# Performance work log

Hardware: AMD Instinct MI355X
Metric: run time of the kernel (lower is better)

## Reference

```python
import jax, jax.numpy as jnp
from jax import lax
import numpy as np

MAX_ITER = 50
BAND_WIDTH = 3.0
MIN_BAND_VOXELS = 32
EPS = 1e-06


def _chamfer(mask_f):
    # mask_f: [N, H, W] float in {0,1}. Iterative 3x3 max-pool dilation; a pixel
    # newly reached at iteration i gets distance i (matches torch max_pool2d loop).
    # Running the full MAX_ITER iterations is equivalent to the early break:
    # once no new pixels appear, dist is never updated again.
    def body(i, carry):
        dist, cur = carry
        dil = lax.reduce_window(cur, -jnp.inf, lax.max, (1, 3, 3), (1, 1, 1), 'SAME')
        new = (dil > 0) & (cur == 0)
        dist = jnp.where(new, i.astype(dist.dtype), dist)
        return (dist, dil)

    dist0 = jnp.zeros_like(mask_f)
    dist, _ = lax.fori_loop(1, MAX_ITER + 1, body, (dist0, mask_f))
    return dist


def _signed_distance(m):
    # m: [N, H, W] float binary masks. Positive outside, negative inside.
    H, W = m.shape[-2], m.shape[-1]
    sdm = _chamfer(m) - _chamfer(1.0 - m)
    msum = m.sum((-2, -1))
    trivial = (msum == 0) | (msum == H * W)  # all-empty or all-full -> zeros
    return jnp.where(trivial[:, None, None], 0.0, sdm)


def setup_inputs() -> dict:
    key = jax.random.key(0)
    k1, k2 = jax.random.split(key)
    B, C, H, W = 8, 4, 512, 512
    probs = jax.random.uniform(k1, (B, C, H, W), dtype=jnp.float32)
    target = jax.random.randint(k2, (B, H, W), 0, C, dtype=jnp.int64)
    return {"probs": probs, "target": target}


def reference(probs, target):
    B, C, H, W = probs.shape
    probs = probs.astype(jnp.float32)
    # one-hot [B, C, H, W] bool; default include_background=False -> classes 1..C-1
    one_hot = target[:, None, :, :] == jnp.arange(C, dtype=target.dtype)[None, :, None, None]
    m = one_hot[:, 1:].astype(jnp.float32).reshape(B * (C - 1), H, W)
    p = probs[:, 1:].reshape(B * (C - 1), H, W)

    d = jnp.abs(_signed_distance(m))          # [N, H, W]
    band = (d <= BAND_WIDTH).astype(jnp.float32)
    denom = band.sum((-2, -1))                 # [N]

    err = jnp.abs(p - m)                       # L1 (error_power=1.0)
    loss_bc = (err * d * band).sum((-2, -1)) / (denom + EPS)

    include = (denom >= MIN_BAND_VOXELS).astype(jnp.float32)
    count = include.sum()
    return (loss_bc * include).sum() / (count + EPS)
```

## Files before the change

kernel.cpp:

```cpp
#include <hip/hip_runtime.h>


#define HH 512
#define WW 512
#define BB 8
#define NCLS 4
#define TILE 32
#define HALO 3
#define LTS (TILE + 2*HALO)
#define LSTRIDE 40
#define NBLK 2048
#define WS2_OFF (9 * NBLK)


__global__ __launch_bounds__(256) void gsl_stage1(
    const float* __restrict__ probs,
    const int*   __restrict__ target,
    float* __restrict__ ws)
{
    __shared__ uint32_t tile[LTS * LSTRIDE];
    __shared__ float redf[4][3];
    __shared__ int   redi[4][3];

    const int b   = blockIdx.z;
    const int gx0 = blockIdx.x * TILE - HALO;
    const int gy0 = blockIdx.y * TILE - HALO;
    const int tid = threadIdx.y * 16 + threadIdx.x;
    const int* __restrict__ tgt_b = target + b * (HH * WW);

    for (int i = tid; i < LTS * LTS; i += 256) {
        int ly = i / LTS, lx = i - ly * LTS;
        int gy = gy0 + ly, gx = gx0 + lx;
        uint32_t bits = 0u;
        if ((unsigned)gy < (unsigned)HH && (unsigned)gx < (unsigned)WW)
            bits = 1u << (uint32_t)tgt_b[gy * WW + gx];
        tile[ly * LSTRIDE + lx] = bits;
    }
    __syncthreads();

    float num[3] = {0.f, 0.f, 0.f};
    int   den[3] = {0, 0, 0};
    int   mc [3] = {0, 0, 0};

    #pragma unroll
    for (int sy = 0; sy < 2; ++sy)
    #pragma unroll
    for (int sx = 0; sx < 2; ++sx) {
        const int px = threadIdx.x + 16 * sx;
        const int py = threadIdx.y + 16 * sy;
        const int lx = px + HALO, ly = py + HALO;
        const int gx = blockIdx.x * TILE + px;
        const int gy = blockIdx.y * TILE + py;

        uint32_t p1 = 0u, p2 = 0u, p3 = 0u;
        #pragma unroll
        for (int dy = -3; dy <= 3; ++dy) {
            #pragma unroll
            for (int dx = -3; dx <= 3; ++dx) {
                uint32_t v = tile[(ly + dy) * LSTRIDE + (lx + dx)];
                const int ady = dy < 0 ? -dy : dy;
                const int adx = dx < 0 ? -dx : dx;
                const int r = ady > adx ? ady : adx;
                if (r <= 1) p1 |= v;
                if (r <= 2) p2 |= v;
                p3 |= v;
            }
        }
        const uint32_t cbits = tile[ly * LSTRIDE + lx];

        #pragma unroll
        for (int k = 0; k < 3; ++k) {
            const int c = k + 1;
            const uint32_t cm = 1u << c;
            const bool v = (cbits & cm) != 0u;
            const bool a1 = v ? ((p1 & ~cm) != 0u) : ((p1 & cm) != 0u);
            const bool a2 = v ? ((p2 & ~cm) != 0u) : ((p2 & cm) != 0u);
            const bool a3 = v ? ((p3 & ~cm) != 0u) : ((p3 & cm) != 0u);
            const int d = a1 ? 1 : (a2 ? 2 : 3);
            const float p = probs[(((b * NCLS) + c) * HH + gy) * WW + gx];
            const float err = fabsf(p - (v ? 1.0f : 0.0f));
            num[k] += a3 ? err * (float)d : 0.0f;
            den[k] += a3 ? 1 : 0;
            mc [k] += v ? 1 : 0;
        }
    }

    int pk0 = den[0] | (den[1] << 16);
    int pk1 = den[2] | (mc[0] << 16);
    int pk2 = mc[1]  | (mc[2] << 16);

    const int lane = tid & 63, wave = tid >> 6;
    #pragma unroll
    for (int off = 32; off; off >>= 1) {
        num[0] += __shfl_down(num[0], off, 64);
        num[1] += __shfl_down(num[1], off, 64);
        num[2] += __shfl_down(num[2], off, 64);
        pk0    += __shfl_down(pk0,    off, 64);
        pk1    += __shfl_down(pk1,    off, 64);
        pk2    += __shfl_down(pk2,    off, 64);
    }
    if (lane == 0) {
        redf[wave][0] = num[0]; redf[wave][1] = num[1]; redf[wave][2] = num[2];
        redi[wave][0] = pk0;    redi[wave][1] = pk1;    redi[wave][2] = pk2;
    }
    __syncthreads();
    if (tid == 0) {
        const int blockFlat = ((b * 16) + blockIdx.y) * 16 + blockIdx.x;
        float n0 = 0.f, n1 = 0.f, n2 = 0.f;
        int s0 = 0, s1 = 0, s2 = 0;
        #pragma unroll
        for (int w = 0; w < 4; ++w) {
            n0 += redf[w][0]; n1 += redf[w][1]; n2 += redf[w][2];
            s0 += redi[w][0]; s1 += redi[w][1]; s2 += redi[w][2];
        }
        ws[(0 * 3 + 0) * NBLK + blockFlat] = n0;
        ws[(0 * 3 + 1) * NBLK + blockFlat] = n1;
        ws[(0 * 3 + 2) * NBLK + blockFlat] = n2;
        ws[(1 * 3 + 0) * NBLK + blockFlat] = (float)(s0 & 0xFFFF);
        ws[(1 * 3 + 1) * NBLK + blockFlat] = (float)(s0 >> 16);
        ws[(1 * 3 + 2) * NBLK + blockFlat] = (float)(s1 & 0xFFFF);
        ws[(2 * 3 + 0) * NBLK + blockFlat] = (float)(s1 >> 16);
        ws[(2 * 3 + 1) * NBLK + blockFlat] = (float)(s2 & 0xFFFF);
        ws[(2 * 3 + 2) * NBLK + blockFlat] = (float)(s2 >> 16);
    }
}

__global__ __launch_bounds__(256) void gsl_stage2(float* __restrict__ ws)
{
    __shared__ float red[4];
    const int g = blockIdx.x;
    const int k = g >> 3, b = g & 7;
    const int tid = threadIdx.x;

    float s = ws[k * NBLK + b * 256 + tid];
    #pragma unroll
    for (int off = 32; off; off >>= 1) s += __shfl_down(s, off, 64);
    if ((tid & 63) == 0) red[tid >> 6] = s;
    __syncthreads();
    if (tid == 0) {
        const int grp = k / 3, cc = k % 3;
        ws[WS2_OFF + grp * 24 + b * 3 + cc] = red[0] + red[1] + red[2] + red[3];
    }
}

__global__ __launch_bounds__(64) void gsl_stage3(
    const float* __restrict__ ws, float* __restrict__ out)
{
    const float* ws2 = ws + WS2_OFF;
    const int n = threadIdx.x;
    float loss = 0.0f, incl = 0.0f;
    if (n < 24) {
        const float num = ws2[n];
        const float den = ws2[24 + n];
        const float mcv = ws2[48 + n];
        const bool trivial = (mcv == 0.0f) || (mcv == (float)(HH * WW));
        if (trivial) {
            incl = 1.0f; loss = 0.0f;
        } else if (den >= 32.0f) {
            incl = 1.0f;
            loss = num / (den + 1e-6f);
        }
    }
    #pragma unroll
    for (int off = 32; off; off >>= 1) {
        loss += __shfl_down(loss, off, 64);
        incl += __shfl_down(incl, off, 64);
    }
    if (n == 0) out[0] = loss / (incl + 1e-6f);
}

extern "C" void kernel_launch(void* const* d_in, const int* in_sizes, int n_in,
                              void* d_out, int out_size, void* d_ws, size_t ws_size,
                              hipStream_t stream)
{
    const float* probs  = (const float*)d_in[0];
    const int*   target = (const int*)d_in[1];
    float* out = (float*)d_out;
    float* ws  = (float*)d_ws;

    dim3 grid1(WW / TILE, HH / TILE, BB);
    dim3 block1(16, 16);
    gsl_stage1<<<grid1, block1, 0, stream>>>(probs, target, ws);
    gsl_stage2<<<72, 256, 0, stream>>>(ws);
    gsl_stage3<<<1, 64, 0, stream>>>(ws, out);
}
```

Baseline: 94.57 us.

## Pack class bitmasks into nibbles and compute band distances with row-wise dilation

Replaces the 2D shared-memory tile with 7x7 neighbourhood ORs by packing 8 pixels' class bits into one 32-bit word per lane. Horizontal 1/2/3-pixel dilations are built with shifts and cross-lane shuffles, and vertical dilation is an OR over rows stored in shared memory. Blocks now process full-width 8-row strips with vectorized int4/float4 loads, and the two reduction kernels are merged into one finishing kernel. The aim is to cut the 49 LDS reads per pixel, the halo overhead and one kernel launch. The cost is more complex bit logic and fewer, larger blocks (512 total).

```diff
diff --git a/kernel.cpp b/kernel.cpp
--- a/kernel.cpp
+++ b/kernel.cpp
@@ -4,13 +4,9 @@
 #define HH 512
 #define WW 512
 #define BB 8
-#define NCLS 4
-#define TILE 32
-#define HALO 3
-#define LTS (TILE + 2*HALO)
-#define LSTRIDE 40
-#define NBLK 2048
-#define WS2_OFF (9 * NBLK)
+#define STRIP 8
+#define SROWS (STRIP + 6)
+#define NBLK 512
 
 
 __global__ __launch_bounds__(256) void gsl_stage1(
@@ -18,23 +14,40 @@
     const int*   __restrict__ target,
     float* __restrict__ ws)
 {
-    __shared__ uint32_t tile[LTS * LSTRIDE];
+    __shared__ uint4 hrow[SROWS * 64];
     __shared__ float redf[4][3];
     __shared__ int   redi[4][3];
 
-    const int b   = blockIdx.z;
-    const int gx0 = blockIdx.x * TILE - HALO;
-    const int gy0 = blockIdx.y * TILE - HALO;
-    const int tid = threadIdx.y * 16 + threadIdx.x;
+    const int tid   = threadIdx.x;
+    const int lane  = tid & 63;
+    const int wave  = tid >> 6;
+    const int strip = blockIdx.x;
+    const int b     = blockIdx.y;
+    const int y0    = strip * STRIP;
     const int* __restrict__ tgt_b = target + b * (HH * WW);
 
-    for (int i = tid; i < LTS * LTS; i += 256) {
-        int ly = i / LTS, lx = i - ly * LTS;
-        int gy = gy0 + ly, gx = gx0 + lx;
-        uint32_t bits = 0u;
-        if ((unsigned)gy < (unsigned)HH && (unsigned)gx < (unsigned)WW)
-            bits = 1u << (uint32_t)tgt_b[gy * WW + gx];
-        tile[ly * LSTRIDE + lx] = bits;
+    #pragma unroll
+    for (int i = 0; i < 4; ++i) {
+        const int ri = wave + 4 * i;
+        if (ri < SROWS) {
+            const int gy = y0 - 3 + ri;
+            uint32_t wv = 0u, h1 = 0u, h2 = 0u, h3 = 0u;
+            if ((unsigned)gy < (unsigned)HH) {
+                const int4* trow = (const int4*)(tgt_b + gy * WW);
+                const int4 t0 = trow[lane * 2];
+                const int4 t1 = trow[lane * 2 + 1];
+                wv = (1u << t0.x)        | (1u << (t0.y + 4))
+                   | (1u << (t0.z + 8))  | (1u << (t0.w + 12))
+                   | (1u << (t1.x + 16)) | (1u << (t1.y + 20))
+                   | (1u << (t1.z + 24)) | (1u << (t1.w + 28));
+                uint32_t wl = __shfl_up(wv, 1, 64);   if (lane == 0)  wl = 0u;
+                uint32_t wr = __shfl_down(wv, 1, 64); if (lane == 63) wr = 0u;
+                h1 = wv | ((wv << 4)  | (wl >> 28)) | ((wv >> 4)  | (wr << 28));
+                h2 = h1 | ((wv << 8)  | (wl >> 24)) | ((wv >> 8)  | (wr << 24));
+                h3 = h2 | ((wv << 12) | (wl >> 20)) | ((wv >> 12) | (wr << 20));
+            }
+            hrow[ri * 64 + lane] = make_uint4(h1, h2, h3, wv);
+        }
     }
     __syncthreads();
 
@@ -43,53 +56,61 @@
     int   mc [3] = {0, 0, 0};
 
     #pragma unroll
-    for (int sy = 0; sy < 2; ++sy)
-    #pragma unroll
-    for (int sx = 0; sx < 2; ++sx) {
-        const int px = threadIdx.x + 16 * sx;
-        const int py = threadIdx.y + 16 * sy;
-        const int lx = px + HALO, ly = py + HALO;
-        const int gx = blockIdx.x * TILE + px;
-        const int gy = blockIdx.y * TILE + py;
-
-        uint32_t p1 = 0u, p2 = 0u, p3 = 0u;
-        #pragma unroll
-        for (int dy = -3; dy <= 3; ++dy) {
+    for (int t = 0; t < 2; ++t) {
+        const int yo = wave * 2 + t;
+        const int gy = y0 + yo;
+        const int lr = yo + 3;
+
+        const float4* pr1 = (const float4*)(probs + (size_t)(((b * 4) + 1) * HH + gy) * WW);
+        const float4* pr2 = (const float4*)(probs + (size_t)(((b * 4) + 2) * HH + gy) * WW);
+        const float4* pr3 = (const float4*)(probs + (size_t)(((b * 4) + 3) * HH + gy) * WW);
+        const float4 f1a = pr1[lane * 2], f1b = pr1[lane * 2 + 1];
+        const float4 f2a = pr2[lane * 2], f2b = pr2[lane * 2 + 1];
+        const float4 f3a = pr3[lane * 2], f3b = pr3[lane * 2 + 1];
+
+        const uint4 r0 = hrow[(lr - 3) * 64 + lane];
+        const uint4 r1 = hrow[(lr - 2) * 64 + lane];
+        const uint4 r2 = hrow[(lr - 1) * 64 + lane];
+        const uint4 r3 = hrow[(lr    ) * 64 + lane];
+        const uint4 r4 = hrow[(lr + 1) * 64 + lane];
+        const uint4 r5 = hrow[(lr + 2) * 64 + lane];
+        const uint4 r6 = hrow[(lr + 3) * 64 + lane];
+        const uint32_t p1 = r2.x | r3.x | r4.x;
+        const uint32_t p2 = r1.y | r2.y | r3.y | r4.y | r5.y;
+        const uint32_t p3 = r0.z | r1.z | r2.z | r3.z | r4.z | r5.z | r6.z;
+        const uint32_t cw = r3.w;
+
+        const float pv[3][8] = {
+            {f1a.x, f1a.y, f1a.z, f1a.w, f1b.x, f1b.y, f1b.z, f1b.w},
+            {f2a.x, f2a.y, f2a.z, f2a.w, f2b.x, f2b.y, f2b.z, f2b.w},
+            {f3a.x, f3a.y, f3a.z, f3a.w, f3b.x, f3b.y, f3b.z, f3b.w}};
+
+        #pragma unroll
+        for (int j = 0; j < 8; ++j) {
+            const uint32_t q1 = (p1 >> (4 * j)) & 15u;
+            const uint32_t q2 = (p2 >> (4 * j)) & 15u;
+            const uint32_t q3 = (p3 >> (4 * j)) & 15u;
+            const uint32_t cb = (cw >> (4 * j)) & 15u;
             #pragma unroll
-            for (int dx = -3; dx <= 3; ++dx) {
-                uint32_t v = tile[(ly + dy) * LSTRIDE + (lx + dx)];
-                const int ady = dy < 0 ? -dy : dy;
-                const int adx = dx < 0 ? -dx : dx;
-                const int r = ady > adx ? ady : adx;
-                if (r <= 1) p1 |= v;
-                if (r <= 2) p2 |= v;
-                p3 |= v;
+            for (int k = 0; k < 3; ++k) {
+                const uint32_t cm = 2u << k;
+                const bool v = (cb & cm) != 0u;
+                const uint32_t sel = v ? (15u & ~cm) : cm;
+                const uint32_t a1 = q1 & sel;
+                const uint32_t a2 = q2 & sel;
+                const uint32_t a3 = q3 & sel;
+                const float df  = a1 ? 1.f : (a2 ? 2.f : 3.f);
+                const float err = fabsf(pv[k][j] - (v ? 1.f : 0.f));
+                num[k] += a3 ? err * df : 0.f;
+                den[k] += a3 ? 1 : 0;
+                mc [k] += v  ? 1 : 0;
             }
-        }
-        const uint32_t cbits = tile[ly * LSTRIDE + lx];
-
-        #pragma unroll
-        for (int k = 0; k < 3; ++k) {
-            const int c = k + 1;
-            const uint32_t cm = 1u << c;
-            const bool v = (cbits & cm) != 0u;
-            const bool a1 = v ? ((p1 & ~cm) != 0u) : ((p1 & cm) != 0u);
-            const bool a2 = v ? ((p2 & ~cm) != 0u) : ((p2 & cm) != 0u);
-            const bool a3 = v ? ((p3 & ~cm) != 0u) : ((p3 & cm) != 0u);
-            const int d = a1 ? 1 : (a2 ? 2 : 3);
-            const float p = probs[(((b * NCLS) + c) * HH + gy) * WW + gx];
-            const float err = fabsf(p - (v ? 1.0f : 0.0f));
-            num[k] += a3 ? err * (float)d : 0.0f;
-            den[k] += a3 ? 1 : 0;
-            mc [k] += v ? 1 : 0;
         }
     }
 
     int pk0 = den[0] | (den[1] << 16);
     int pk1 = den[2] | (mc[0] << 16);
     int pk2 = mc[1]  | (mc[2] << 16);
-
-    const int lane = tid & 63, wave = tid >> 6;
     #pragma unroll
     for (int off = 32; off; off >>= 1) {
         num[0] += __shfl_down(num[0], off, 64);
@@ -105,7 +126,7 @@
     }
     __syncthreads();
     if (tid == 0) {
-        const int blockFlat = ((b * 16) + blockIdx.y) * 16 + blockIdx.x;
+        const int blockFlat = b * 64 + strip;
         float n0 = 0.f, n1 = 0.f, n2 = 0.f;
         int s0 = 0, s1 = 0, s2 = 0;
         #pragma unroll
@@ -125,48 +146,43 @@
     }
 }
 
-__global__ __launch_bounds__(256) void gsl_stage2(float* __restrict__ ws)
-{
-    __shared__ float red[4];
-    const int g = blockIdx.x;
-    const int k = g >> 3, b = g & 7;
-    const int tid = threadIdx.x;
-
-    float s = ws[k * NBLK + b * 256 + tid];
-    #pragma unroll
-    for (int off = 32; off; off >>= 1) s += __shfl_down(s, off, 64);
-    if ((tid & 63) == 0) red[tid >> 6] = s;
-    __syncthreads();
-    if (tid == 0) {
-        const int grp = k / 3, cc = k % 3;
-        ws[WS2_OFF + grp * 24 + b * 3 + cc] = red[0] + red[1] + red[2] + red[3];
-    }
-}
-
-__global__ __launch_bounds__(64) void gsl_stage3(
+__global__ __launch_bounds__(1024) void gsl_finish(
     const float* __restrict__ ws, float* __restrict__ out)
 {
-    const float* ws2 = ws + WS2_OFF;
-    const int n = threadIdx.x;
-    float loss = 0.0f, incl = 0.0f;
-    if (n < 24) {
-        const float num = ws2[n];
-        const float den = ws2[24 + n];
-        const float mcv = ws2[48 + n];
-        const bool trivial = (mcv == 0.0f) || (mcv == (float)(HH * WW));
-        if (trivial) {
-            incl = 1.0f; loss = 0.0f;
-        } else if (den >= 32.0f) {
-            incl = 1.0f;
-            loss = num / (den + 1e-6f);
-        }
-    }
-    #pragma unroll
-    for (int off = 32; off; off >>= 1) {
-        loss += __shfl_down(loss, off, 64);
-        incl += __shfl_down(incl, off, 64);
-    }
-    if (n == 0) out[0] = loss / (incl + 1e-6f);
+    __shared__ float ws2[72];
+    const int tid = threadIdx.x, lane = tid & 63, wave = tid >> 6;
+
+    for (int g = wave; g < 72; g += 16) {
+        const int grp = g / 24, rem = g - grp * 24;
+        const int bb = rem / 3, cc = rem - bb * 3;
+        float s = ws[(grp * 3 + cc) * NBLK + bb * 64 + lane];
+        #pragma unroll
+        for (int off = 32; off; off >>= 1) s += __shfl_down(s, off, 64);
+        if (lane == 0) ws2[g] = s;
+    }
+    __syncthreads();
+
+    if (wave == 0) {
+        float loss = 0.f, incl = 0.f;
+        if (lane < 24) {
+            const float num = ws2[lane];
+            const float den = ws2[24 + lane];
+            const float mcv = ws2[48 + lane];
+            const bool trivial = (mcv == 0.f) || (mcv == (float)(HH * WW));
+            if (trivial) {
+                incl = 1.f; loss = 0.f;
+            } else if (den >= 32.f) {
+                incl = 1.f;
+                loss = num / (den + 1e-6f);
+            }
+        }
+        #pragma unroll
+        for (int off = 32; off; off >>= 1) {
+            loss += __shfl_down(loss, off, 64);
+            incl += __shfl_down(incl, off, 64);
+        }
+        if (lane == 0) out[0] = loss / (incl + 1e-6f);
+    }
 }
 
 extern "C" void kernel_launch(void* const* d_in, const int* in_sizes, int n_in,
@@ -178,9 +194,7 @@
     float* out = (float*)d_out;
     float* ws  = (float*)d_ws;
 
-    dim3 grid1(WW / TILE, HH / TILE, BB);
-    dim3 block1(16, 16);
-    gsl_stage1<<<grid1, block1, 0, stream>>>(probs, target, ws);
-    gsl_stage2<<<72, 256, 0, stream>>>(ws);
-    gsl_stage3<<<1, 64, 0, stream>>>(ws, out);
+    dim3 grid1(64, BB);
+    gsl_stage1<<<grid1, 256, 0, stream>>>(probs, target, ws);
+    gsl_finish<<<1, 1024, 0, stream>>>(ws, out);
 }
```

After: 84.81 us (median of 2 runs). -10.3%, faster.
